# Kernel optimization log

Measured on AMD Instinct MI355X. Metric: run time of the kernel, lower is better.

## Reference

```python
import jax, jax.numpy as jnp
import numpy as np

IN_FEATURES = 2048
OUT_FEATURES = 8192


def setup_inputs() -> dict:
    key = jax.random.key(0)
    k_x, k_w, k_s, k_b = jax.random.split(key, 4)
    x = jax.random.normal(k_x, (4, 2048, IN_FEATURES), dtype=jnp.float32)
    # int8 weights as produced by quantize(): values in [-128, 127]
    weight_int8 = jax.random.randint(k_w, (OUT_FEATURES, IN_FEATURES), -128, 128, dtype=jnp.int8)
    # per-output-row scale, shape [out_features, 1]
    scale = jax.random.uniform(k_s, (OUT_FEATURES, 1), dtype=jnp.float32, minval=1e-4, maxval=0.02)
    bias = jax.random.normal(k_b, (OUT_FEATURES,), dtype=jnp.float32) * 0.01
    return {"x": x, "weight_int8": weight_int8, "scale": scale, "bias": bias}


def reference(x, weight_int8, scale, bias):
    # dequantize: [out, in] int8 -> x.dtype, scaled per output row
    weight = weight_int8.astype(x.dtype) * scale.astype(x.dtype)
    # F.linear: x @ weight.T + bias
    return jnp.einsum('bsi,oi->bso', x, weight) + bias.astype(x.dtype)
```

## Files before the change

### kernel.cpp

```cpp
#include <hip/hip_runtime.h>
#include <hip/hip_bf16.h>

#define M_DIM 8192
#define N_DIM 8192
#define K_DIM 2048

#define BK 64
#define NT (K_DIM / BK)
#define SLOT_BYTES 32768

typedef float f32x4 __attribute__((ext_vector_type(4)));
typedef int   i32x4 __attribute__((ext_vector_type(4)));
typedef unsigned int u32;
typedef u32 u32x2 __attribute__((ext_vector_type(2)));
typedef u32 u32x4 __attribute__((ext_vector_type(4)));


__device__ __forceinline__ void gload16(const unsigned char* g, char* l) {
    __builtin_amdgcn_global_load_lds(
        (const __attribute__((address_space(1))) u32*)g,
        (__attribute__((address_space(3))) u32*)l, 16, 0, 0);
}

__device__ __forceinline__ u32 pack4(int a, int b, int c, int d) {
    return (u32)(a & 255) | ((u32)(b & 255) << 8) |
           ((u32)(c & 255) << 16) | ((u32)(d & 255) << 24);
}


__global__ void __launch_bounds__(256) quant_x_k(const float* __restrict__ x,
                                                 unsigned char* __restrict__ xq,
                                                 float* __restrict__ sx) {
    const int row = blockIdx.x;
    const int t = threadIdx.x;
    const float* xr = x + (size_t)row * K_DIM;
    f32x4 v0 = *((const f32x4*)xr + t * 2);
    f32x4 v1 = *((const f32x4*)xr + t * 2 + 1);
    float m = fabsf(v0[0]);
    m = fmaxf(m, fabsf(v0[1])); m = fmaxf(m, fabsf(v0[2])); m = fmaxf(m, fabsf(v0[3]));
    m = fmaxf(m, fabsf(v1[0])); m = fmaxf(m, fabsf(v1[1]));
    m = fmaxf(m, fabsf(v1[2])); m = fmaxf(m, fabsf(v1[3]));
#pragma unroll
    for (int off = 32; off >= 1; off >>= 1)
        m = fmaxf(m, __shfl_xor(m, off, 64));
    __shared__ float wmax[4];
    if ((t & 63) == 0) wmax[t >> 6] = m;
    __syncthreads();
    m = fmaxf(fmaxf(wmax[0], wmax[1]), fmaxf(wmax[2], wmax[3]));
    m = fmaxf(m, 1e-20f);
    const float rs = 127.0f / m;
    const int q0 = (int)rintf(v0[0] * rs), q1 = (int)rintf(v0[1] * rs);
    const int q2 = (int)rintf(v0[2] * rs), q3 = (int)rintf(v0[3] * rs);
    const int q4 = (int)rintf(v1[0] * rs), q5 = (int)rintf(v1[1] * rs);
    const int q6 = (int)rintf(v1[2] * rs), q7 = (int)rintf(v1[3] * rs);
    u32x2 o;
    o[0] = pack4(q0, q1, q2, q3);
    o[1] = pack4(q4, q5, q6, q7);
    *((u32x2*)(xq + (size_t)row * K_DIM) + t) = o;
    if (t == 0) sx[row] = m / 127.0f;
}


__global__ void __launch_bounds__(256) cvt_w_k(const int* __restrict__ w,
                                               unsigned char* __restrict__ wq, int n16) {
    const int stride = gridDim.x * blockDim.x;
    for (int i = blockIdx.x * blockDim.x + threadIdx.x; i < n16; i += stride) {
        const i32x4* p = (const i32x4*)w + (size_t)i * 4;
        i32x4 a = p[0], b = p[1], c = p[2], d = p[3];
        u32x4 o;
        o[0] = pack4(a[0], a[1], a[2], a[3]);
        o[1] = pack4(b[0], b[1], b[2], b[3]);
        o[2] = pack4(c[0], c[1], c[2], c[3]);
        o[3] = pack4(d[0], d[1], d[2], d[3]);
        *((u32x4*)wq + i) = o;
    }
}


__global__ void __launch_bounds__(512, 2)
gemm_i8(const unsigned char* __restrict__ Aq, const unsigned char* __restrict__ Bq,
        const float* __restrict__ sx, const float* __restrict__ sw,
        const float* __restrict__ bias, float* __restrict__ C) {
    extern __shared__ __align__(16) char ldsb[];

    const int bid = blockIdx.x;
    const int swz = (bid & 7) * 128 + (bid >> 3);
    const int rowBase = (swz >> 5) * 256;
    const int colBase = (swz & 31) * 256;

    const int t = threadIdx.x;
    const int l = t & 63;
    const int w = t >> 6;
    const int wm = w >> 2;
    const int wn = w & 3;
    const int fr = l & 15;
    const int s4 = l >> 4;

    const int sr = t >> 2;
    const int sk = (((t & 3) ^ ((sr >> 1) & 3)) * 16);
    const unsigned char* gA0 = Aq + (size_t)(rowBase + sr) * K_DIM + sk;
    const unsigned char* gA1 = Aq + (size_t)(rowBase + 128 + sr) * K_DIM + sk;
    const unsigned char* gB0 = Bq + (size_t)(colBase + sr) * K_DIM + sk;
    const unsigned char* gB1 = Bq + (size_t)(colBase + 128 + sr) * K_DIM + sk;

#define STAGE(tk) do { \
        char* _b = ldsb + ((tk) & 3) * SLOT_BYTES; \
        const int _k = (tk) * BK; \
        gload16(gA0 + _k, _b + t * 16); \
        gload16(gA1 + _k, _b + 8192 + t * 16); \
        gload16(gB0 + _k, _b + 16384 + t * 16); \
        gload16(gB1 + _k, _b + 24576 + t * 16); \
    } while (0)

    const int pc = ((s4 ^ ((fr >> 1) & 3)) * 16);
    int aoff[8], boff[4];
#pragma unroll
    for (int mi = 0; mi < 8; ++mi)
        aoff[mi] = (wm * 128 + mi * 16 + fr) * 64 + pc;
#pragma unroll
    for (int ni = 0; ni < 4; ++ni)
        boff[ni] = 16384 + (wn * 64 + ni * 16 + fr) * 64 + pc;

    i32x4 acc[8][4] = {};
    i32x4 afC[8], bf0[4], bf1[4];

#define SB    __builtin_amdgcn_sched_barrier(0)
#define BAR   __builtin_amdgcn_s_barrier()
#define P1    __builtin_amdgcn_s_setprio(1)
#define P0    __builtin_amdgcn_s_setprio(0)
#define LGKM0 asm volatile("s_waitcnt lgkmcnt(0)" ::: "memory")
#define VM8   asm volatile("s_waitcnt vmcnt(8)" ::: "memory")
#define VM4   asm volatile("s_waitcnt vmcnt(4)" ::: "memory")
#define VM0   asm volatile("s_waitcnt vmcnt(0)" ::: "memory")

#define READS_B(dst, tk) do { \
        const char* _s = ldsb + ((tk) & 3) * SLOT_BYTES; \
        _Pragma("unroll") \
        for (int ni = 0; ni < 4; ++ni) dst[ni] = *(const i32x4*)(_s + boff[ni]); \
    } while (0)
#define READS_A(tk) do { \
        const char* _s = ldsb + ((tk) & 3) * SLOT_BYTES; \
        _Pragma("unroll") \
        for (int mi = 0; mi < 8; ++mi) afC[mi] = *(const i32x4*)(_s + aoff[mi]); \
    } while (0)

#define MFMA_ILV(BREG, NTK) do { P1; \
        const char* _n = ldsb + ((NTK) & 3) * SLOT_BYTES; \
        _Pragma("unroll") \
        for (int mi = 0; mi < 8; ++mi) { \
            _Pragma("unroll") \
            for (int ni = 0; ni < 4; ++ni) \
                acc[mi][ni] = __builtin_amdgcn_mfma_i32_16x16x64_i8( \
                    afC[mi], BREG[ni], acc[mi][ni], 0, 0, 0); \
            afC[mi] = *(const i32x4*)(_n + aoff[mi]); \
        } \
        P0; } while (0)

#define MFMA_ALL(BREG) do { P1; \
        _Pragma("unroll") \
        for (int mi = 0; mi < 8; ++mi) \
            _Pragma("unroll") \
            for (int ni = 0; ni < 4; ++ni) \
                acc[mi][ni] = __builtin_amdgcn_mfma_i32_16x16x64_i8( \
                    afC[mi], BREG[ni], acc[mi][ni], 0, 0, 0); \
        P0; } while (0)

#define BODY(TK, BCUR, BNXT) do { \
        STAGE((TK) + 3); \
        VM8; LGKM0; SB; BAR; SB; \
        READS_B(BNXT, (TK) + 1); \
        MFMA_ILV(BCUR, (TK) + 1); \
    } while (0)

    STAGE(0); STAGE(1); STAGE(2);
    VM8; SB; BAR; SB;
    READS_B(bf0, 0); READS_A(0);

#pragma unroll 1
    for (int tk = 0; tk < NT - 4; tk += 2) {
        BODY(tk, bf0, bf1);
        BODY(tk + 1, bf1, bf0);
    }
    BODY(28, bf0, bf1);
    VM4; LGKM0; SB; BAR; SB;
    READS_B(bf0, 30);
    MFMA_ILV(bf1, 30);
    VM0; LGKM0; SB; BAR; SB;
    READS_B(bf1, 31);
    MFMA_ILV(bf0, 31);
    LGKM0; SB;
    MFMA_ALL(bf1);

#undef BODY
#undef MFMA_ALL
#undef MFMA_ILV
#undef READS_A
#undef READS_B
#undef STAGE

#pragma unroll
    for (int ni = 0; ni < 4; ++ni) {
        const int col = colBase + wn * 64 + ni * 16 + fr;
        const float swc = sw[col];
        const float bz = bias[col];
#pragma unroll
        for (int mi = 0; mi < 8; ++mi) {
            const int rb = rowBase + wm * 128 + mi * 16 + s4 * 4;
            i32x4 a = acc[mi][ni];
#pragma unroll
            for (int r = 0; r < 4; ++r)
                C[(size_t)(rb + r) * N_DIM + col] =
                    (float)a[r] * (sx[rb + r] * swc) + bz;
        }
    }
}


typedef int i32x4_t __attribute__((ext_vector_type(4)));
__global__ void __launch_bounds__(256) naive_k(const float* __restrict__ x,
                                               const int* __restrict__ w,
                                               const float* __restrict__ scale,
                                               const float* __restrict__ bias,
                                               float* __restrict__ out) {
    __shared__ float xs[K_DIM];
    const int m = blockIdx.x >> 5;
    const int n = ((blockIdx.x & 31) << 8) + threadIdx.x;
    for (int i = threadIdx.x; i < K_DIM; i += 256) xs[i] = x[(size_t)m * K_DIM + i];
    __syncthreads();
    const int* wr = w + (size_t)n * K_DIM;
    float acc = 0.f;
    for (int k = 0; k < K_DIM; k += 4) {
        i32x4_t v = *(const i32x4_t*)(wr + k);
        acc += xs[k]     * (float)v[0];
        acc += xs[k + 1] * (float)v[1];
        acc += xs[k + 2] * (float)v[2];
        acc += xs[k + 3] * (float)v[3];
    }
    out[(size_t)m * N_DIM + n] = acc * scale[n] + bias[n];
}


extern "C" void kernel_launch(void* const* d_in, const int* in_sizes, int n_in,
                              void* d_out, int out_size, void* d_ws, size_t ws_size,
                              hipStream_t stream) {
    const float* x     = (const float*)d_in[0];
    const int*   w8    = (const int*)d_in[1];
    const float* sw    = (const float*)d_in[2];
    const float* bias  = (const float*)d_in[3];
    float*       out   = (float*)d_out;

    const size_t xq_bytes = (size_t)M_DIM * K_DIM;
    const size_t wq_bytes = (size_t)N_DIM * K_DIM;
    const size_t need = xq_bytes + wq_bytes + (size_t)M_DIM * sizeof(float);
    if (ws_size >= need) {
        unsigned char* xq = (unsigned char*)d_ws;
        unsigned char* wq = xq + xq_bytes;
        float* sx = (float*)(wq + wq_bytes);
        hipFuncSetAttribute((const void*)gemm_i8,
                            hipFuncAttributeMaxDynamicSharedMemorySize, 131072);
        quant_x_k<<<M_DIM, 256, 0, stream>>>(x, xq, sx);
        cvt_w_k<<<2048, 256, 0, stream>>>(w8, wq, N_DIM * K_DIM / 16);
        gemm_i8<<<dim3((M_DIM / 256) * (N_DIM / 256)), 512, 131072, stream>>>(
            xq, wq, sx, sw, bias, out);
    } else {
        naive_k<<<(M_DIM * (N_DIM / 256)), 256, 0, stream>>>(x, w8, sw, bias, out);
    }
}
```

Measured before the change: 220.0 us.

## Load B fragments directly from global into registers, bypassing LDS

The B (weight) tile is no longer staged through LDS. Each wave loads its own B fragments from global memory straight into registers one k-step ahead, which halves the LDS slot size and the dynamic shared memory. This is meant to cut LDS traffic and footprint, which may allow more blocks per CU. The cost is that B data shared by the two wm waves is fetched twice from global/L2, and the loads are uncoalesced strided 16-byte reads with less prefetch distance than the old 3-stage LDS pipeline.

```diff
diff --git a/kernel.cpp b/kernel.cpp
--- a/kernel.cpp
+++ b/kernel.cpp
@@ -7,7 +7,7 @@
 
 #define BK 64
 #define NT (K_DIM / BK)
-#define SLOT_BYTES 32768
+#define SLOT_BYTES 16384
 
 typedef float f32x4 __attribute__((ext_vector_type(4)));
 typedef int   i32x4 __attribute__((ext_vector_type(4)));
@@ -100,26 +100,28 @@
     const int sk = (((t & 3) ^ ((sr >> 1) & 3)) * 16);
     const unsigned char* gA0 = Aq + (size_t)(rowBase + sr) * K_DIM + sk;
     const unsigned char* gA1 = Aq + (size_t)(rowBase + 128 + sr) * K_DIM + sk;
-    const unsigned char* gB0 = Bq + (size_t)(colBase + sr) * K_DIM + sk;
-    const unsigned char* gB1 = Bq + (size_t)(colBase + 128 + sr) * K_DIM + sk;
-
-#define STAGE(tk) do { \
+
+#define STAGE_A(tk) do { \
         char* _b = ldsb + ((tk) & 3) * SLOT_BYTES; \
         const int _k = (tk) * BK; \
         gload16(gA0 + _k, _b + t * 16); \
         gload16(gA1 + _k, _b + 8192 + t * 16); \
-        gload16(gB0 + _k, _b + 16384 + t * 16); \
-        gload16(gB1 + _k, _b + 24576 + t * 16); \
+    } while (0)
+
+    const unsigned char* gBf = Bq + (size_t)(colBase + wn * 64 + fr) * K_DIM + s4 * 16;
+
+#define BLOAD(dst, tk) do { \
+        const unsigned char* _g = gBf + (size_t)(tk) * BK; \
+        _Pragma("unroll") \
+        for (int ni = 0; ni < 4; ++ni) \
+            dst[ni] = *(const i32x4*)(_g + (size_t)ni * 16 * K_DIM); \
     } while (0)
 
     const int pc = ((s4 ^ ((fr >> 1) & 3)) * 16);
-    int aoff[8], boff[4];
+    int aoff[8];
 #pragma unroll
     for (int mi = 0; mi < 8; ++mi)
         aoff[mi] = (wm * 128 + mi * 16 + fr) * 64 + pc;
-#pragma unroll
-    for (int ni = 0; ni < 4; ++ni)
-        boff[ni] = 16384 + (wn * 64 + ni * 16 + fr) * 64 + pc;
 
     i32x4 acc[8][4] = {};
     i32x4 afC[8], bf0[4], bf1[4];
@@ -129,15 +131,11 @@
 #define P1    __builtin_amdgcn_s_setprio(1)
 #define P0    __builtin_amdgcn_s_setprio(0)
 #define LGKM0 asm volatile("s_waitcnt lgkmcnt(0)" ::: "memory")
-#define VM8   asm volatile("s_waitcnt vmcnt(8)" ::: "memory")
+#define VM6   asm volatile("s_waitcnt vmcnt(6)" ::: "memory")
 #define VM4   asm volatile("s_waitcnt vmcnt(4)" ::: "memory")
+#define VM2   asm volatile("s_waitcnt vmcnt(2)" ::: "memory")
 #define VM0   asm volatile("s_waitcnt vmcnt(0)" ::: "memory")
 
-#define READS_B(dst, tk) do { \
-        const char* _s = ldsb + ((tk) & 3) * SLOT_BYTES; \
-        _Pragma("unroll") \
-        for (int ni = 0; ni < 4; ++ni) dst[ni] = *(const i32x4*)(_s + boff[ni]); \
-    } while (0)
 #define READS_A(tk) do { \
         const char* _s = ldsb + ((tk) & 3) * SLOT_BYTES; \
         _Pragma("unroll") \
@@ -166,15 +164,17 @@
         P0; } while (0)
 
 #define BODY(TK, BCUR, BNXT) do { \
-        STAGE((TK) + 3); \
-        VM8; LGKM0; SB; BAR; SB; \
-        READS_B(BNXT, (TK) + 1); \
+        STAGE_A((TK) + 3); \
+        BLOAD(BNXT, (TK) + 1); \
+        VM6; LGKM0; SB; BAR; SB; \
         MFMA_ILV(BCUR, (TK) + 1); \
     } while (0)
 
-    STAGE(0); STAGE(1); STAGE(2);
-    VM8; SB; BAR; SB;
-    READS_B(bf0, 0); READS_A(0);
+    STAGE_A(0); STAGE_A(1);
+    BLOAD(bf0, 0);
+    STAGE_A(2);
+    VM2; SB; BAR; SB;
+    READS_A(0);
 
 #pragma unroll 1
     for (int tk = 0; tk < NT - 4; tk += 2) {
@@ -182,21 +182,21 @@
         BODY(tk + 1, bf1, bf0);
     }
     BODY(28, bf0, bf1);
+    BLOAD(bf0, 30);
     VM4; LGKM0; SB; BAR; SB;
-    READS_B(bf0, 30);
     MFMA_ILV(bf1, 30);
-    VM0; LGKM0; SB; BAR; SB;
-    READS_B(bf1, 31);
+    BLOAD(bf1, 31);
+    VM4; LGKM0; SB; BAR; SB;
     MFMA_ILV(bf0, 31);
-    LGKM0; SB;
+    VM0; LGKM0; SB;
     MFMA_ALL(bf1);
 
 #undef BODY
 #undef MFMA_ALL
 #undef MFMA_ILV
 #undef READS_A
-#undef READS_B
-#undef STAGE
+#undef BLOAD
+#undef STAGE_A
 
 #pragma unroll
     for (int ni = 0; ni < 4; ++ni) {
@@ -257,10 +257,10 @@
         unsigned char* wq = xq + xq_bytes;
         float* sx = (float*)(wq + wq_bytes);
         hipFuncSetAttribute((const void*)gemm_i8,
-                            hipFuncAttributeMaxDynamicSharedMemorySize, 131072);
+                            hipFuncAttributeMaxDynamicSharedMemorySize, 65536);
         quant_x_k<<<M_DIM, 256, 0, stream>>>(x, xq, sx);
         cvt_w_k<<<2048, 256, 0, stream>>>(w8, wq, N_DIM * K_DIM / 16);
-        gemm_i8<<<dim3((M_DIM / 256) * (N_DIM / 256)), 512, 131072, stream>>>(
+        gemm_i8<<<dim3((M_DIM / 256) * (N_DIM / 256)), 512, 65536, stream>>>(
             xq, wq, sx, sw, bias, out);
     } else {
         naive_k<<<(M_DIM * (N_DIM / 256)), 256, 0, stream>>>(x, w8, sw, bias, out);
```

New measurement: 247.2 us. 12.4% more time.
